# Kernel tuning notes

Measured on AMD Instinct MI355X. Metric: run time of the kernel, lower is better.

## Reference

```python
import jax, jax.numpy as jnp
import numpy as np

N = 50000      # n_nodes
E = 800000     # n_edges
F_IN = 128     # raw feature dim
H = 64         # hidden_channels
L = 2          # max_hash_hops / num GCN layers
NUM_PERM = 128 # minhash permutations
HLL_M = 64     # 2**hll_p registers


def setup_inputs() -> dict:
    key = jax.random.key(0)
    ks = jax.random.split(key, 8)
    x = jax.random.normal(ks[0], (N, F_IN), jnp.float32)
    edge_index = jax.random.randint(ks[1], (2, E), 0, N, dtype=jnp.int32)
    minhash0 = jax.random.randint(ks[2], (N, NUM_PERM), 0, 2147483647, dtype=jnp.int32)
    hll0 = jax.random.randint(ks[3], (N, HLL_M), 0, 20, dtype=jnp.int32)
    W_enc = jax.random.normal(ks[4], (F_IN, H), jnp.float32) / np.sqrt(F_IN)
    b_enc = jnp.zeros((H,), jnp.float32)
    W_convs = jax.random.normal(ks[5], (L, H, H), jnp.float32) / np.sqrt(H)
    b_convs = jnp.zeros((L, H), jnp.float32)
    return {"x": x, "edge_index": edge_index, "minhash0": minhash0, "hll0": hll0,
            "W_enc": W_enc, "b_enc": b_enc, "W_convs": W_convs, "b_convs": b_convs}


def _hll_count(hll):
    # standard HyperLogLog estimator: alpha_m * m^2 / sum(2^-reg)
    m = hll.shape[1]
    alpha = 0.7213 / (1.0 + 1.079 / m)
    s = jnp.sum(jnp.exp2(-hll.astype(jnp.float32)), axis=1)  # [N]
    return alpha * m * m / s


def reference(x, edge_index, minhash0, hll0, W_enc, b_enc, W_convs, b_convs):
    src, dst = edge_index[0], edge_index[1]
    loops = jnp.arange(N, dtype=src.dtype)
    # add_self_loops: used for both hash propagation and (internally) by GCNConv
    src_sl = jnp.concatenate([src, loops])  # [E+N]
    dst_sl = jnp.concatenate([dst, loops])

    # gcn_norm: D^-1/2 (A+I) D^-1/2 with degrees counted on self-looped graph
    deg = jax.ops.segment_sum(jnp.ones_like(dst_sl, jnp.float32), dst_sl, num_segments=N)
    dis = jnp.where(deg > 0, jax.lax.rsqrt(jnp.maximum(deg, 1.0)), 0.0)
    norm = dis[src_sl] * dis[dst_sl]  # [E+N]

    # k=0: feature encoder (dropout off in eval)
    h = x @ W_enc + b_enc  # [N, H]

    mh, hll = minhash0, hll0
    cards = []
    for k in range(L):
        # hash propagation: HLL = register-wise max over neighborhood,
        # minhash = permutation-wise min over neighborhood (self-looped graph)
        hll = jax.ops.segment_max(hll[src_sl], dst_sl, num_segments=N)
        mh = jax.ops.segment_min(mh[src_sl], dst_sl, num_segments=N)
        cards.append(_hll_count(hll))
        # GCNConv: gather - (x W) - scatter with symmetric norm, then residual
        msg = (h @ W_convs[k])[src_sl] * norm[:, None]  # [E+N, H]
        out = jax.ops.segment_sum(msg, dst_sl, num_segments=N) + b_convs[k]
        h = h + out  # feature_prop == 'residual' (dropout off)

    cards = jnp.stack(cards, axis=1)  # [N, L]
    return h, cards, mh, hll
```

## Files before the change

kernel.cpp:

```cpp
#include <hip/hip_runtime.h>
#include <hip/hip_bf16.h>

typedef unsigned int uint;
typedef unsigned short ushort;

#define N_NODES 50000
#define N_EDGES 800000
#define FDIM 128
#define HID 64
#define NPERM 128
#define HLLM 64
#define DUMMY 50000

#define BSHIFT 8
#define BNODES 256
#define NBUCK 196
#define CAPB 6144
#define SCAT_BLOCKS 256
#define EDGES_PER_BLK 3125
#define MH_BLOCKS 12500
#define HLL_BLOCKS 3125
#define SLICE_CAP 8448
#define CONV_BLOCKS 782

__device__ __forceinline__ uint pk_min_u16(uint a, uint b) {
    uint d;
    asm("v_pk_min_u16 %0, %1, %2" : "=v"(d) : "v"(a), "v"(b));
    return d;
}


__device__ __forceinline__ void mh_body(int node, uint l, const int2* __restrict__ off2,
                                        const ushort* __restrict__ csr,
                                        const uint* __restrict__ mh_in,
                                        uint* __restrict__ out_p, float* __restrict__ out_f) {
    int2 se = off2[node];
    uint mnA = 0xFFFFFFFFu, mnB = 0xFFFFFFFFu, mnC = 0xFFFFFFFFu, mnD = 0xFFFFFFFFu;
    for (int p = se.x; p < se.y; p += 8) {
        uint4 c4 = *(const uint4*)(csr + p);
        uint j0 = c4.x & 0xFFFFu, j1 = c4.x >> 16;
        uint j2 = c4.y & 0xFFFFu, j3 = c4.y >> 16;
        uint j4 = c4.z & 0xFFFFu, j5 = c4.z >> 16;
        uint j6 = c4.w & 0xFFFFu, j7 = c4.w >> 16;
        uint a0 = mh_in[j0 * 64u + l];
        uint a1 = mh_in[j1 * 64u + l];
        uint a2 = mh_in[j2 * 64u + l];
        uint a3 = mh_in[j3 * 64u + l];
        uint a4 = mh_in[j4 * 64u + l];
        uint a5 = mh_in[j5 * 64u + l];
        uint a6 = mh_in[j6 * 64u + l];
        uint a7 = mh_in[j7 * 64u + l];
        mnA = pk_min_u16(mnA, a0); mnB = pk_min_u16(mnB, a1);
        mnC = pk_min_u16(mnC, a2); mnD = pk_min_u16(mnD, a3);
        mnA = pk_min_u16(mnA, a4); mnB = pk_min_u16(mnB, a5);
        mnC = pk_min_u16(mnC, a6); mnD = pk_min_u16(mnD, a7);
    }
    mnA = pk_min_u16(pk_min_u16(mnA, mnB), pk_min_u16(mnC, mnD));
    uint mn0 = mnA & 0xFFFFu, mn1 = mnA >> 16;
    if (out_p) {
        out_p[(size_t)node * 64 + l] = mn0 | (mn1 << 16);
    } else {
        float2 w;
        w.x = __uint_as_float(mn0 << 16);
        w.y = __uint_as_float(mn1 << 16);
        *(float2*)(out_f + (size_t)node * NPERM + 2 * l) = w;
    }
}

__device__ __forceinline__ void hll_body(int node, uint q, const int2* __restrict__ off2,
                                         const ushort* __restrict__ csr,
                                         const uint* __restrict__ hll_in,
                                         uint* __restrict__ out_p, float* __restrict__ out_f,
                                         float* __restrict__ cards, int kcol) {
    int2 se = off2[node];
    uint m0 = 0, m1 = 0, m2 = 0, m3 = 0;
#define HLL_ACC(vv) do { uint _v = (vv); \
        m0 = max(m0, _v & 0xFFu); m1 = max(m1, (_v >> 8) & 0xFFu); \
        m2 = max(m2, (_v >> 16) & 0xFFu); m3 = max(m3, _v >> 24); } while (0)
    for (int p = se.x; p < se.y; p += 8) {
        uint4 c4 = *(const uint4*)(csr + p);
        uint j0 = c4.x & 0xFFFFu, j1 = c4.x >> 16;
        uint j2 = c4.y & 0xFFFFu, j3 = c4.y >> 16;
        uint j4 = c4.z & 0xFFFFu, j5 = c4.z >> 16;
        uint j6 = c4.w & 0xFFFFu, j7 = c4.w >> 16;
        uint a0 = hll_in[j0 * 16u + q];
        uint a1 = hll_in[j1 * 16u + q];
        uint a2 = hll_in[j2 * 16u + q];
        uint a3 = hll_in[j3 * 16u + q];
        uint a4 = hll_in[j4 * 16u + q];
        uint a5 = hll_in[j5 * 16u + q];
        uint a6 = hll_in[j6 * 16u + q];
        uint a7 = hll_in[j7 * 16u + q];
        HLL_ACC(a0); HLL_ACC(a1); HLL_ACC(a2); HLL_ACC(a3);
        HLL_ACC(a4); HLL_ACC(a5); HLL_ACC(a6); HLL_ACC(a7);
    }
#undef HLL_ACC
    if (out_p) out_p[(size_t)node * 16 + q] = m0 | (m1 << 8) | (m2 << 16) | (m3 << 24);
    if (out_f) {
        float4 w = {(float)m0, (float)m1, (float)m2, (float)m3};
        *(float4*)(out_f + (size_t)node * HLLM + 4 * q) = w;
    }
    float v = exp2f(-(float)m0) + exp2f(-(float)m1) + exp2f(-(float)m2) + exp2f(-(float)m3);
    v += __shfl_xor(v, 1); v += __shfl_xor(v, 2);
    v += __shfl_xor(v, 4); v += __shfl_xor(v, 8);
    if (q == 0) {
        const float alphamm = (float)(0.7213 / (1.0 + 1.079 / 64.0) * 64.0 * 64.0);
        cards[(size_t)node * 2 + kcol] = alphamm / v;
    }
}

__device__ __forceinline__ void agg_body(int node, uint c, const int2* __restrict__ off2,
                                         const ushort* __restrict__ csr,
                                         const ushort* __restrict__ hWs,
                                         const float* __restrict__ dis,
                                         const float* __restrict__ b,
                                         const float* __restrict__ h_in,
                                         float* __restrict__ h_out) {
    int2 se = off2[node];
    float acc0 = 0.f, acc1 = 0.f;
    for (int p = se.x; p < se.y; p += 8) {
        uint4 c4 = *(const uint4*)(csr + p);
        uint j0 = c4.x & 0xFFFFu, j1 = c4.x >> 16;
        uint j2 = c4.y & 0xFFFFu, j3 = c4.y >> 16;
        uint j4 = c4.z & 0xFFFFu, j5 = c4.z >> 16;
        uint j6 = c4.w & 0xFFFFu, j7 = c4.w >> 16;
        uint a0 = hWs[j0 * 64u + c];
        uint a1 = hWs[j1 * 64u + c];
        uint a2 = hWs[j2 * 64u + c];
        uint a3 = hWs[j3 * 64u + c];
        uint a4 = hWs[j4 * 64u + c];
        uint a5 = hWs[j5 * 64u + c];
        uint a6 = hWs[j6 * 64u + c];
        uint a7 = hWs[j7 * 64u + c];
        acc0 += __uint_as_float(a0 << 16) + __uint_as_float(a1 << 16)
              + __uint_as_float(a2 << 16) + __uint_as_float(a3 << 16);
        acc1 += __uint_as_float(a4 << 16) + __uint_as_float(a5 << 16)
              + __uint_as_float(a6 << 16) + __uint_as_float(a7 << 16);
    }
    float acc = acc0 + acc1;
    h_out[(size_t)node * HID + c] = h_in[(size_t)node * HID + c] + b[c] + dis[node] * acc;
}

__device__ __forceinline__ void convmm_body(int row, int c0, const float* __restrict__ h,
                                            const float* __restrict__ Ws,
                                            const float* __restrict__ dis,
                                            ushort* __restrict__ hWs) {
    float acc[16] = {0.f, 0.f, 0.f, 0.f, 0.f, 0.f, 0.f, 0.f,
                     0.f, 0.f, 0.f, 0.f, 0.f, 0.f, 0.f, 0.f};
    const float4* hr = (const float4*)(h + (size_t)row * HID);
    for (int k4 = 0; k4 < HID / 4; ++k4) {
        float4 hv = hr[k4];
        const float* wr = Ws + (k4 * 4) * HID + c0;
#pragma unroll
        for (int j = 0; j < 16; ++j) acc[j] = fmaf(hv.x, wr[j], acc[j]);
#pragma unroll
        for (int j = 0; j < 16; ++j) acc[j] = fmaf(hv.y, wr[HID + j], acc[j]);
#pragma unroll
        for (int j = 0; j < 16; ++j) acc[j] = fmaf(hv.z, wr[2 * HID + j], acc[j]);
#pragma unroll
        for (int j = 0; j < 16; ++j) acc[j] = fmaf(hv.w, wr[3 * HID + j], acc[j]);
    }
    float d = dis[row];
    ushort* o = hWs + (size_t)row * HID + c0;
#pragma unroll
    for (int j = 0; j < 16; ++j) {
        __hip_bfloat16 t = __float2bfloat16(d * acc[j]);
        o[j] = *(ushort*)&t;
    }
}


__global__ void __launch_bounds__(256) k_pack(const int* __restrict__ mh, uint* __restrict__ mhp,
                       uint* __restrict__ mhA,
                       const int* __restrict__ hll, uint* __restrict__ hp,
                       uint* __restrict__ hllA,
                       int* __restrict__ gcur, int* __restrict__ pcur) {
    int b = blockIdx.x;
    if (b < MH_BLOCKS) {
        int i = b * 256 + threadIdx.x;
        int2 v = ((const int2*)mh)[i];
        uint u0 = __float_as_uint((float)v.x) >> 16;
        uint u1 = __float_as_uint((float)v.y) >> 16;
        mhp[i] = u0 | (u1 << 16);
    } else if (b < MH_BLOCKS + HLL_BLOCKS) {
        int i = (b - MH_BLOCKS) * 256 + threadIdx.x;
        int4 v = ((const int4*)hll)[i];
        hp[i] = (uint)v.x | ((uint)v.y << 8) | ((uint)v.z << 16) | ((uint)v.w << 24);
    } else {
        int t = threadIdx.x;
        if (t < NBUCK) gcur[t] = t * CAPB;
        if (t == 255) pcur[0] = 0;
        if (t < 64) {
            mhp[(size_t)DUMMY * 64 + t] = 0xFFFFFFFFu;
            mhA[(size_t)DUMMY * 64 + t] = 0xFFFFFFFFu;
        } else if (t < 80) {
            hp[(size_t)DUMMY * 16 + (t - 64)] = 0u;
        } else if (t < 96) {
            hllA[(size_t)DUMMY * 16 + (t - 80)] = 0u;
        }
    }
}


__global__ void __launch_bounds__(256) k_enc(const float* __restrict__ x,
                       const float* __restrict__ W_enc, const float* __restrict__ b_enc,
                       float* __restrict__ h) {
    __shared__ float smem[FDIM * HID];
    for (int idx = threadIdx.x; idx < FDIM * HID; idx += 256) smem[idx] = W_enc[idx];
    __syncthreads();
    int row = blockIdx.x * 64 + (threadIdx.x >> 2);
    int c0 = (threadIdx.x & 3) * 16;
    if (row >= N_NODES) return;
    float acc[16];
#pragma unroll
    for (int j = 0; j < 16; ++j) acc[j] = b_enc[c0 + j];
    const float4* xr = (const float4*)(x + (size_t)row * FDIM);
    for (int k4 = 0; k4 < FDIM / 4; ++k4) {
        float4 xv = xr[k4];
        const float* wr = smem + (k4 * 4) * HID + c0;
#pragma unroll
        for (int j = 0; j < 16; ++j) acc[j] = fmaf(xv.x, wr[j], acc[j]);
#pragma unroll
        for (int j = 0; j < 16; ++j) acc[j] = fmaf(xv.y, wr[HID + j], acc[j]);
#pragma unroll
        for (int j = 0; j < 16; ++j) acc[j] = fmaf(xv.z, wr[2 * HID + j], acc[j]);
#pragma unroll
        for (int j = 0; j < 16; ++j) acc[j] = fmaf(xv.w, wr[3 * HID + j], acc[j]);
    }
    float* hr = h + (size_t)row * HID + c0;
#pragma unroll
    for (int j = 0; j < 16; ++j) hr[j] = acc[j];
}


__global__ void __launch_bounds__(256) k_scatter(const int* __restrict__ src,
                          const int* __restrict__ dst,
                          int* __restrict__ gcur, uint* __restrict__ ebuf) {
    __shared__ uint ecache[EDGES_PER_BLK];
    __shared__ int cnt[NBUCK];
    __shared__ int cur[NBUCK];
    int t = threadIdx.x;
    for (int i = t; i < NBUCK; i += 256) cnt[i] = 0;
    __syncthreads();
    int e0 = blockIdx.x * EDGES_PER_BLK;
    for (int i = t; i < EDGES_PER_BLK; i += 256) {
        int d = dst[e0 + i];
        int s = src[e0 + i];
        ecache[i] = ((uint)s << 16) | (uint)d;
        atomicAdd(&cnt[d >> BSHIFT], 1);
    }
    __syncthreads();
    for (int b = t; b < NBUCK; b += 256)
        cur[b] = atomicAdd(&gcur[b], cnt[b]);
    __syncthreads();
    for (int i = t; i < EDGES_PER_BLK; i += 256) {
        uint en = ecache[i];
        uint d = en & 0xFFFFu;
        int p = atomicAdd(&cur[d >> BSHIFT], 1);
        ebuf[p] = ((en >> 16) << BSHIFT) | (d & (BNODES - 1));
    }
}


__global__ void __launch_bounds__(256) k_csr(const uint* __restrict__ ebuf,
                      const int* __restrict__ gcur, int* __restrict__ pcur,
                      int2* __restrict__ off2, float* __restrict__ dis,
                      ushort* __restrict__ csr) {
    __shared__ int lcur[BNODES];
    __shared__ int ssum[256];
    __shared__ uint slice[SLICE_CAP];
    __shared__ int sbase;
    int b = blockIdx.x;
    int lo = b << BSHIFT;
    int nbkt = min(BNODES, N_NODES - lo);
    int ebase = b * CAPB;
    int ecnt = gcur[b] - ebase;
    int t = threadIdx.x;
    lcur[t] = 0;
    __syncthreads();
    for (int i = t; i < ecnt; i += 256)
        atomicAdd(&lcur[ebuf[ebase + i] & (BNODES - 1)], 1);
    __syncthreads();
    int a0 = lcur[t];
    int plen = (t < nbkt) ? ((a0 + 8) & ~7) : 0;
    ssum[t] = plen;
    __syncthreads();
    for (int off = 1; off < 256; off <<= 1) {
        int u = (t >= off) ? ssum[t - off] : 0;
        __syncthreads();
        ssum[t] += u;
        __syncthreads();
    }
    int ppre = ssum[t] - plen;
    if (t == 255) sbase = atomicAdd(pcur, ssum[255]);
    __syncthreads();
    int base = sbase;
    if (t < nbkt) {
        slice[ppre] = (uint)(lo + t);
        lcur[t] = ppre + 1;
        off2[lo + t] = make_int2(base + ppre, base + ppre + plen);
        dis[lo + t] = rsqrtf((float)(a0 + 1));
    }
    __syncthreads();
    for (int i = t; i < ecnt; i += 256) {
        uint en = ebuf[ebase + i];
        int p = atomicAdd(&lcur[en & (BNODES - 1)], 1);
        slice[p] = en >> BSHIFT;
    }
    __syncthreads();
    if (t < nbkt)
        for (int i = lcur[t]; i < ppre + plen; ++i) slice[i] = DUMMY;
    __syncthreads();
    int total = ssum[255];
    for (int i = t; i < total; i += 256) csr[base + i] = (ushort)slice[i];
}


__global__ void __launch_bounds__(256) k_hopA(const int2* __restrict__ off2,
                    const ushort* __restrict__ csr,
                    const uint* __restrict__ mh_in, uint* __restrict__ mh_out_p,
                    const uint* __restrict__ hll_in, uint* __restrict__ hll_out_p,
                    float* __restrict__ cards,
                    const float* __restrict__ h, const float* __restrict__ W,
                    const float* __restrict__ dis, ushort* __restrict__ hWs) {
    __shared__ float Ws[HID * HID];
    int blk = blockIdx.x;
    if (blk < MH_BLOCKS) {
        int node = blk * 4 + (threadIdx.x >> 6);
        mh_body(node, threadIdx.x & 63, off2, csr, mh_in, mh_out_p, nullptr);
    } else if (blk < MH_BLOCKS + HLL_BLOCKS) {
        int node = (blk - MH_BLOCKS) * 16 + (threadIdx.x >> 4);
        hll_body(node, threadIdx.x & 15, off2, csr, hll_in, hll_out_p, nullptr, cards, 0);
    } else {
        for (int i = threadIdx.x; i < HID * HID; i += 256) Ws[i] = W[i];
        __syncthreads();
        int row = (blk - MH_BLOCKS - HLL_BLOCKS) * 64 + (threadIdx.x >> 2);
        int c0 = (threadIdx.x & 3) * 16;
        if (row > N_NODES) return;
        if (row == N_NODES) {
            ushort* o = hWs + (size_t)row * HID + c0;
#pragma unroll
            for (int j = 0; j < 16; ++j) o[j] = 0;
            return;
        }
        convmm_body(row, c0, h, Ws, dis, hWs);
    }
}


__global__ void __launch_bounds__(256) k_hopB(const int2* __restrict__ off2,
                    const ushort* __restrict__ csr,
                    const uint* __restrict__ mh_in, float* __restrict__ mh_out_f,
                    const ushort* __restrict__ hWs, const float* __restrict__ b0,
                    float* __restrict__ h_cur,
                    const uint* __restrict__ hll_in, float* __restrict__ hll_out_f,
                    float* __restrict__ cards, const float* __restrict__ dis) {
    int blk = blockIdx.x;
    if (blk < MH_BLOCKS) {
        int node = blk * 4 + (threadIdx.x >> 6);
        mh_body(node, threadIdx.x & 63, off2, csr, mh_in, nullptr, mh_out_f);
    } else if (blk < 2 * MH_BLOCKS) {
        int node = (blk - MH_BLOCKS) * 4 + (threadIdx.x >> 6);
        agg_body(node, threadIdx.x & 63, off2, csr, hWs, dis, b0, h_cur, h_cur);
    } else {
        int node = (blk - 2 * MH_BLOCKS) * 16 + (threadIdx.x >> 4);
        hll_body(node, threadIdx.x & 15, off2, csr, hll_in, nullptr, hll_out_f, cards, 1);
    }
}


__global__ void __launch_bounds__(256) k_conv(const float* __restrict__ h,
                         const float* __restrict__ W, const float* __restrict__ dis,
                         ushort* __restrict__ hWs) {
    __shared__ float Ws[HID * HID];
    for (int i = threadIdx.x; i < HID * HID; i += 256) Ws[i] = W[i];
    __syncthreads();
    int row = blockIdx.x * 64 + (threadIdx.x >> 2);
    int c0 = (threadIdx.x & 3) * 16;
    if (row > N_NODES) return;
    if (row == N_NODES) {
        ushort* o = hWs + (size_t)row * HID + c0;
#pragma unroll
        for (int j = 0; j < 16; ++j) o[j] = 0;
        return;
    }
    convmm_body(row, c0, h, Ws, dis, hWs);
}


__global__ void __launch_bounds__(256) k_agg(const int2* __restrict__ off2,
                      const ushort* __restrict__ csr, const ushort* __restrict__ hWs,
                      const float* __restrict__ dis, const float* __restrict__ b,
                      const float* __restrict__ h_in, float* __restrict__ h_out) {
    int node = blockIdx.x * 4 + (threadIdx.x >> 6);
    agg_body(node, threadIdx.x & 63, off2, csr, hWs, dis, b, h_in, h_out);
}


static inline char* align256(char* p) {
    return (char*)(((uintptr_t)p + 255) & ~(uintptr_t)255);
}

extern "C" void kernel_launch(void* const* d_in, const int* in_sizes, int n_in,
                              void* d_out, int out_size, void* d_ws, size_t ws_size,
                              hipStream_t stream) {
    const float* x       = (const float*)d_in[0];
    const int*   ei      = (const int*)d_in[1];
    const int*   mh0     = (const int*)d_in[2];
    const int*   hll0    = (const int*)d_in[3];
    const float* W_enc   = (const float*)d_in[4];
    const float* b_enc   = (const float*)d_in[5];
    const float* W_convs = (const float*)d_in[6];
    const float* b_convs = (const float*)d_in[7];

    float* out       = (float*)d_out;
    float* out_h     = out;
    float* out_cards = out + (size_t)N_NODES * HID;
    float* out_mh    = out_cards + (size_t)N_NODES * 2;
    float* out_hll   = out_mh + (size_t)N_NODES * NPERM;

    char* w = (char*)d_ws;
    int*   gcur    = (int*)w;   w = align256(w + (size_t)NBUCK * 4);
    int*   pcur    = (int*)w;   w = align256(w + 4);
    int2*  off2    = (int2*)w;  w = align256(w + (size_t)N_NODES * 8);
    float* dis     = (float*)w; w = align256(w + (size_t)N_NODES * 4);
    ushort* csr    = (ushort*)w; w = align256(w + (size_t)(N_EDGES + 8 * N_NODES) * 2);
    uint*  mhp0    = (uint*)w;  w = align256(w + (size_t)(N_NODES + 1) * 64 * 4);
    uint*  mhA     = (uint*)w;  w = align256(w + (size_t)(N_NODES + 1) * 64 * 4);
    uint*  hp0     = (uint*)w;  w = align256(w + (size_t)(N_NODES + 1) * 16 * 4);
    uint*  hllA    = (uint*)w;  w = align256(w + (size_t)(N_NODES + 1) * 16 * 4);
    float* h_cur   = (float*)w; w = align256(w + (size_t)N_NODES * HID * 4);
    ushort* hWs    = (ushort*)w; w = align256(w + (size_t)(N_NODES + 1) * HID * 2);
    uint*  ebuf    = mhA;

    const int* src = ei;
    const int* dst = ei + N_EDGES;

    k_pack<<<MH_BLOCKS + HLL_BLOCKS + 1, 256, 0, stream>>>(
        mh0, mhp0, mhA, hll0, hp0, hllA, gcur, pcur);
    k_scatter<<<SCAT_BLOCKS, 256, 0, stream>>>(src, dst, gcur, ebuf);
    k_csr<<<NBUCK, 256, 0, stream>>>(ebuf, gcur, pcur, off2, dis, csr);
    k_enc<<<CONV_BLOCKS, 256, 0, stream>>>(x, W_enc, b_enc, h_cur);

    k_hopA<<<MH_BLOCKS + HLL_BLOCKS + CONV_BLOCKS + 1, 256, 0, stream>>>(
        off2, csr, mhp0, mhA, hp0, hllA, out_cards, h_cur, W_convs, dis, hWs);
    k_hopB<<<2 * MH_BLOCKS + HLL_BLOCKS, 256, 0, stream>>>(
        off2, csr, mhA, out_mh, hWs, b_convs, h_cur, hllA, out_hll, out_cards, dis);
    k_conv<<<CONV_BLOCKS + 1, 256, 0, stream>>>(h_cur, W_convs + HID * HID, dis, hWs);
    k_agg<<<MH_BLOCKS, 256, 0, stream>>>(off2, csr, hWs, dis, b_convs + HID, h_cur, out_h);
}
```

Measured before the change: 201.9 us.

## Merge setup kernels into two launches and unroll neighbor-gather loops

Four setup kernels (pack, scatter, CSR build, encoder) become two fused launches: scatter runs alongside the hash packing, and CSR build shares a launch with the feature-encoder GEMM. The bucket cursors are now zeroed with a memset and hold counts instead of absolute offsets, which removes the init dependency inside the pack kernel. The gather loops in the minhash, HLL and aggregation bodies get unroll-2 pragmas to put more loads in flight. This cuts launch count and idle gaps between kernels, at the cost of heterogeneous blocks and a higher shared-memory footprint in the fused kernel, which can lower occupancy for the encoder blocks.

```diff
diff --git a/kernel.cpp b/kernel.cpp
--- a/kernel.cpp
+++ b/kernel.cpp
@@ -36,6 +36,7 @@
                                         uint* __restrict__ out_p, float* __restrict__ out_f) {
     int2 se = off2[node];
     uint mnA = 0xFFFFFFFFu, mnB = 0xFFFFFFFFu, mnC = 0xFFFFFFFFu, mnD = 0xFFFFFFFFu;
+#pragma unroll 2
     for (int p = se.x; p < se.y; p += 8) {
         uint4 c4 = *(const uint4*)(csr + p);
         uint j0 = c4.x & 0xFFFFu, j1 = c4.x >> 16;
@@ -77,6 +78,7 @@
 #define HLL_ACC(vv) do { uint _v = (vv); \
         m0 = max(m0, _v & 0xFFu); m1 = max(m1, (_v >> 8) & 0xFFu); \
         m2 = max(m2, (_v >> 16) & 0xFFu); m3 = max(m3, _v >> 24); } while (0)
+#pragma unroll 2
     for (int p = se.x; p < se.y; p += 8) {
         uint4 c4 = *(const uint4*)(csr + p);
         uint j0 = c4.x & 0xFFFFu, j1 = c4.x >> 16;
@@ -118,6 +120,7 @@
                                          float* __restrict__ h_out) {
     int2 se = off2[node];
     float acc0 = 0.f, acc1 = 0.f;
+#pragma unroll 2
     for (int p = se.x; p < se.y; p += 8) {
         uint4 c4 = *(const uint4*)(csr + p);
         uint j0 = c4.x & 0xFFFFu, j1 = c4.x >> 16;
@@ -170,26 +173,49 @@
 }
 
 
-__global__ void __launch_bounds__(256) k_pack(const int* __restrict__ mh, uint* __restrict__ mhp,
+__global__ void __launch_bounds__(256) k_front(const int* __restrict__ src,
+                       const int* __restrict__ dst, int* __restrict__ gcur,
+                       uint* __restrict__ ebuf,
+                       const int* __restrict__ mh, uint* __restrict__ mhp,
                        uint* __restrict__ mhA,
                        const int* __restrict__ hll, uint* __restrict__ hp,
-                       uint* __restrict__ hllA,
-                       int* __restrict__ gcur, int* __restrict__ pcur) {
+                       uint* __restrict__ hllA) {
+    __shared__ uint ecache[EDGES_PER_BLK];
+    __shared__ int cnt[NBUCK];
+    __shared__ int cur[NBUCK];
     int b = blockIdx.x;
-    if (b < MH_BLOCKS) {
-        int i = b * 256 + threadIdx.x;
+    int t = threadIdx.x;
+    if (b < SCAT_BLOCKS) {
+        for (int i = t; i < NBUCK; i += 256) cnt[i] = 0;
+        __syncthreads();
+        int e0 = b * EDGES_PER_BLK;
+        for (int i = t; i < EDGES_PER_BLK; i += 256) {
+            int d = dst[e0 + i];
+            int s = src[e0 + i];
+            ecache[i] = ((uint)s << 16) | (uint)d;
+            atomicAdd(&cnt[d >> BSHIFT], 1);
+        }
+        __syncthreads();
+        for (int bb = t; bb < NBUCK; bb += 256)
+            cur[bb] = bb * CAPB + atomicAdd(&gcur[bb], cnt[bb]);
+        __syncthreads();
+        for (int i = t; i < EDGES_PER_BLK; i += 256) {
+            uint en = ecache[i];
+            uint d = en & 0xFFFFu;
+            int p = atomicAdd(&cur[d >> BSHIFT], 1);
+            ebuf[p] = ((en >> 16) << BSHIFT) | (d & (BNODES - 1));
+        }
+    } else if (b < SCAT_BLOCKS + MH_BLOCKS) {
+        int i = (b - SCAT_BLOCKS) * 256 + t;
         int2 v = ((const int2*)mh)[i];
         uint u0 = __float_as_uint((float)v.x) >> 16;
         uint u1 = __float_as_uint((float)v.y) >> 16;
         mhp[i] = u0 | (u1 << 16);
-    } else if (b < MH_BLOCKS + HLL_BLOCKS) {
-        int i = (b - MH_BLOCKS) * 256 + threadIdx.x;
+    } else if (b < SCAT_BLOCKS + MH_BLOCKS + HLL_BLOCKS) {
+        int i = (b - SCAT_BLOCKS - MH_BLOCKS) * 256 + t;
         int4 v = ((const int4*)hll)[i];
         hp[i] = (uint)v.x | ((uint)v.y << 8) | ((uint)v.z << 16) | ((uint)v.w << 24);
     } else {
-        int t = threadIdx.x;
-        if (t < NBUCK) gcur[t] = t * CAPB;
-        if (t == 255) pcur[0] = 0;
         if (t < 64) {
             mhp[(size_t)DUMMY * 64 + t] = 0xFFFFFFFFu;
             mhA[(size_t)DUMMY * 64 + t] = 0xFFFFFFFFu;
@@ -202,117 +228,88 @@
 }
 
 
-__global__ void __launch_bounds__(256) k_enc(const float* __restrict__ x,
-                       const float* __restrict__ W_enc, const float* __restrict__ b_enc,
-                       float* __restrict__ h) {
-    __shared__ float smem[FDIM * HID];
-    for (int idx = threadIdx.x; idx < FDIM * HID; idx += 256) smem[idx] = W_enc[idx];
-    __syncthreads();
-    int row = blockIdx.x * 64 + (threadIdx.x >> 2);
-    int c0 = (threadIdx.x & 3) * 16;
-    if (row >= N_NODES) return;
-    float acc[16];
-#pragma unroll
-    for (int j = 0; j < 16; ++j) acc[j] = b_enc[c0 + j];
-    const float4* xr = (const float4*)(x + (size_t)row * FDIM);
-    for (int k4 = 0; k4 < FDIM / 4; ++k4) {
-        float4 xv = xr[k4];
-        const float* wr = smem + (k4 * 4) * HID + c0;
-#pragma unroll
-        for (int j = 0; j < 16; ++j) acc[j] = fmaf(xv.x, wr[j], acc[j]);
-#pragma unroll
-        for (int j = 0; j < 16; ++j) acc[j] = fmaf(xv.y, wr[HID + j], acc[j]);
-#pragma unroll
-        for (int j = 0; j < 16; ++j) acc[j] = fmaf(xv.z, wr[2 * HID + j], acc[j]);
-#pragma unroll
-        for (int j = 0; j < 16; ++j) acc[j] = fmaf(xv.w, wr[3 * HID + j], acc[j]);
-    }
-    float* hr = h + (size_t)row * HID + c0;
-#pragma unroll
-    for (int j = 0; j < 16; ++j) hr[j] = acc[j];
-}
-
-
-__global__ void __launch_bounds__(256) k_scatter(const int* __restrict__ src,
-                          const int* __restrict__ dst,
-                          int* __restrict__ gcur, uint* __restrict__ ebuf) {
-    __shared__ uint ecache[EDGES_PER_BLK];
-    __shared__ int cnt[NBUCK];
-    __shared__ int cur[NBUCK];
-    int t = threadIdx.x;
-    for (int i = t; i < NBUCK; i += 256) cnt[i] = 0;
-    __syncthreads();
-    int e0 = blockIdx.x * EDGES_PER_BLK;
-    for (int i = t; i < EDGES_PER_BLK; i += 256) {
-        int d = dst[e0 + i];
-        int s = src[e0 + i];
-        ecache[i] = ((uint)s << 16) | (uint)d;
-        atomicAdd(&cnt[d >> BSHIFT], 1);
-    }
-    __syncthreads();
-    for (int b = t; b < NBUCK; b += 256)
-        cur[b] = atomicAdd(&gcur[b], cnt[b]);
-    __syncthreads();
-    for (int i = t; i < EDGES_PER_BLK; i += 256) {
-        uint en = ecache[i];
-        uint d = en & 0xFFFFu;
-        int p = atomicAdd(&cur[d >> BSHIFT], 1);
-        ebuf[p] = ((en >> 16) << BSHIFT) | (d & (BNODES - 1));
-    }
-}
-
-
-__global__ void __launch_bounds__(256) k_csr(const uint* __restrict__ ebuf,
+__global__ void __launch_bounds__(256) k_fat1(const uint* __restrict__ ebuf,
                       const int* __restrict__ gcur, int* __restrict__ pcur,
                       int2* __restrict__ off2, float* __restrict__ dis,
-                      ushort* __restrict__ csr) {
-    __shared__ int lcur[BNODES];
-    __shared__ int ssum[256];
-    __shared__ uint slice[SLICE_CAP];
-    __shared__ int sbase;
+                      ushort* __restrict__ csr,
+                      const float* __restrict__ x, const float* __restrict__ W_enc,
+                      const float* __restrict__ b_enc, float* __restrict__ h) {
+    __shared__ uint smem[SLICE_CAP + BNODES + 256 + 1];
     int b = blockIdx.x;
-    int lo = b << BSHIFT;
-    int nbkt = min(BNODES, N_NODES - lo);
-    int ebase = b * CAPB;
-    int ecnt = gcur[b] - ebase;
     int t = threadIdx.x;
-    lcur[t] = 0;
-    __syncthreads();
-    for (int i = t; i < ecnt; i += 256)
-        atomicAdd(&lcur[ebuf[ebase + i] & (BNODES - 1)], 1);
-    __syncthreads();
-    int a0 = lcur[t];
-    int plen = (t < nbkt) ? ((a0 + 8) & ~7) : 0;
-    ssum[t] = plen;
-    __syncthreads();
-    for (int off = 1; off < 256; off <<= 1) {
-        int u = (t >= off) ? ssum[t - off] : 0;
-        __syncthreads();
-        ssum[t] += u;
-        __syncthreads();
-    }
-    int ppre = ssum[t] - plen;
-    if (t == 255) sbase = atomicAdd(pcur, ssum[255]);
-    __syncthreads();
-    int base = sbase;
-    if (t < nbkt) {
-        slice[ppre] = (uint)(lo + t);
-        lcur[t] = ppre + 1;
-        off2[lo + t] = make_int2(base + ppre, base + ppre + plen);
-        dis[lo + t] = rsqrtf((float)(a0 + 1));
-    }
-    __syncthreads();
-    for (int i = t; i < ecnt; i += 256) {
-        uint en = ebuf[ebase + i];
-        int p = atomicAdd(&lcur[en & (BNODES - 1)], 1);
-        slice[p] = en >> BSHIFT;
-    }
-    __syncthreads();
-    if (t < nbkt)
-        for (int i = lcur[t]; i < ppre + plen; ++i) slice[i] = DUMMY;
-    __syncthreads();
-    int total = ssum[255];
-    for (int i = t; i < total; i += 256) csr[base + i] = (ushort)slice[i];
+    if (b < NBUCK) {
+        uint* slice = smem;
+        int* lcur = (int*)(smem + SLICE_CAP);
+        int* ssum = (int*)(smem + SLICE_CAP + BNODES);
+        int* sbase = (int*)(smem + SLICE_CAP + BNODES + 256);
+        int lo = b << BSHIFT;
+        int nbkt = min(BNODES, N_NODES - lo);
+        int ebase = b * CAPB;
+        int ecnt = gcur[b];
+        lcur[t] = 0;
+        __syncthreads();
+        for (int i = t; i < ecnt; i += 256)
+            atomicAdd(&lcur[ebuf[ebase + i] & (BNODES - 1)], 1);
+        __syncthreads();
+        int a0 = lcur[t];
+        int plen = (t < nbkt) ? ((a0 + 8) & ~7) : 0;
+        ssum[t] = plen;
+        __syncthreads();
+        for (int off = 1; off < 256; off <<= 1) {
+            int u = (t >= off) ? ssum[t - off] : 0;
+            __syncthreads();
+            ssum[t] += u;
+            __syncthreads();
+        }
+        int ppre = ssum[t] - plen;
+        if (t == 255) sbase[0] = atomicAdd(pcur, ssum[255]);
+        __syncthreads();
+        int base = sbase[0];
+        if (t < nbkt) {
+            slice[ppre] = (uint)(lo + t);
+            lcur[t] = ppre + 1;
+            off2[lo + t] = make_int2(base + ppre, base + ppre + plen);
+            dis[lo + t] = rsqrtf((float)(a0 + 1));
+        }
+        __syncthreads();
+        for (int i = t; i < ecnt; i += 256) {
+            uint en = ebuf[ebase + i];
+            int p = atomicAdd(&lcur[en & (BNODES - 1)], 1);
+            slice[p] = en >> BSHIFT;
+        }
+        __syncthreads();
+        if (t < nbkt)
+            for (int i = lcur[t]; i < ppre + plen; ++i) slice[i] = DUMMY;
+        __syncthreads();
+        int total = ssum[255];
+        for (int i = t; i < total; i += 256) csr[base + i] = (ushort)slice[i];
+    } else {
+        float* Ws = (float*)smem;
+        for (int idx = t; idx < FDIM * HID; idx += 256) Ws[idx] = W_enc[idx];
+        __syncthreads();
+        int row = (b - NBUCK) * 64 + (t >> 2);
+        int c0 = (t & 3) * 16;
+        if (row >= N_NODES) return;
+        float acc[16];
+#pragma unroll
+        for (int j = 0; j < 16; ++j) acc[j] = b_enc[c0 + j];
+        const float4* xr = (const float4*)(x + (size_t)row * FDIM);
+        for (int k4 = 0; k4 < FDIM / 4; ++k4) {
+            float4 xv = xr[k4];
+            const float* wr = Ws + (k4 * 4) * HID + c0;
+#pragma unroll
+            for (int j = 0; j < 16; ++j) acc[j] = fmaf(xv.x, wr[j], acc[j]);
+#pragma unroll
+            for (int j = 0; j < 16; ++j) acc[j] = fmaf(xv.y, wr[HID + j], acc[j]);
+#pragma unroll
+            for (int j = 0; j < 16; ++j) acc[j] = fmaf(xv.z, wr[2 * HID + j], acc[j]);
+#pragma unroll
+            for (int j = 0; j < 16; ++j) acc[j] = fmaf(xv.w, wr[3 * HID + j], acc[j]);
+        }
+        float* hr = h + (size_t)row * HID + c0;
+#pragma unroll
+        for (int j = 0; j < 16; ++j) hr[j] = acc[j];
+    }
 }
 
 
@@ -420,7 +417,7 @@
     float* out_hll   = out_mh + (size_t)N_NODES * NPERM;
 
     char* w = (char*)d_ws;
-    int*   gcur    = (int*)w;   w = align256(w + (size_t)NBUCK * 4);
+    int*   gcur    = (int*)w;   w += (size_t)NBUCK * 4;
     int*   pcur    = (int*)w;   w = align256(w + 4);
     int2*  off2    = (int2*)w;  w = align256(w + (size_t)N_NODES * 8);
     float* dis     = (float*)w; w = align256(w + (size_t)N_NODES * 4);
@@ -436,11 +433,11 @@
     const int* src = ei;
     const int* dst = ei + N_EDGES;
 
-    k_pack<<<MH_BLOCKS + HLL_BLOCKS + 1, 256, 0, stream>>>(
-        mh0, mhp0, mhA, hll0, hp0, hllA, gcur, pcur);
-    k_scatter<<<SCAT_BLOCKS, 256, 0, stream>>>(src, dst, gcur, ebuf);
-    k_csr<<<NBUCK, 256, 0, stream>>>(ebuf, gcur, pcur, off2, dis, csr);
-    k_enc<<<CONV_BLOCKS, 256, 0, stream>>>(x, W_enc, b_enc, h_cur);
+    hipMemsetAsync(gcur, 0, (size_t)(NBUCK + 1) * 4, stream);
+    k_front<<<SCAT_BLOCKS + MH_BLOCKS + HLL_BLOCKS + 1, 256, 0, stream>>>(
+        src, dst, gcur, ebuf, mh0, mhp0, mhA, hll0, hp0, hllA);
+    k_fat1<<<NBUCK + CONV_BLOCKS, 256, 0, stream>>>(
+        ebuf, gcur, pcur, off2, dis, csr, x, W_enc, b_enc, h_cur);
 
     k_hopA<<<MH_BLOCKS + HLL_BLOCKS + CONV_BLOCKS + 1, 256, 0, stream>>>(
         off2, csr, mhp0, mhA, hp0, hllA, out_cards, h_cur, W_convs, dis, hWs);
```

Result: faster. 184.8 us (-8.5%).
